# Performance work log

Hardware: AMD Instinct MI355X
Metric: run time of the kernel (lower is better)

The kernel has to match this reference:

```python
import jax, jax.numpy as jnp
import numpy as np

MAX_RADIUS = 0.2
MIN_RADIUS = 0.0
SAMPLE_NUM = 32
CHANNEL = 64
EPS = 1e-5


def _ball_query(points, centers):
    """points (B,N,3), centers (B,M,3) -> idx (B,M,S) int32.
    Mimics pointnet2 ball_query: first SAMPLE_NUM point indices within
    [MIN_RADIUS, MAX_RADIUS); slots past the last found repeat the first
    found index (0 if the ball is empty)."""
    d2 = jnp.sum((centers[:, :, None, :] - points[:, None, :, :]) ** 2, axis=-1)  # (B,M,N)
    mask = (d2 < MAX_RADIUS ** 2) & (d2 >= MIN_RADIUS ** 2)
    N = points.shape[1]
    scores = jnp.where(mask, jnp.arange(N, dtype=jnp.int32), jnp.int32(N))
    neg_vals, _ = jax.lax.top_k(-scores, SAMPLE_NUM)  # k smallest indices
    idx = -neg_vals  # (B,M,S), invalid slots == N
    first = idx[..., :1]
    first = jnp.where(first == N, 0, first)
    idx = jnp.where(idx == N, first, idx)
    return idx


def setup_inputs() -> dict:
    key = jax.random.key(0)
    k1, k2, k3, k4 = jax.random.split(key, 4)
    B, N, M, C = 4, 16384, 2048, CHANNEL
    return {
        "points_xyz": jax.random.uniform(k1, (B, N, 3), dtype=jnp.float32),
        "center_xyz": jax.random.uniform(k2, (B, M, 3), dtype=jnp.float32),
        "center_feature": jax.random.normal(k3, (B, M, C), dtype=jnp.float32),
        "features": jax.random.normal(k4, (B, C, N), dtype=jnp.float32),
        "affine_alpha": jnp.ones((1, 1, 1, C + 3), dtype=jnp.float32),
        "affine_beta": jnp.zeros((1, 1, 1, C + 3), dtype=jnp.float32),
    }


def reference(points_xyz, center_xyz, center_feature, features, affine_alpha, affine_beta):
    idx = _ball_query(points_xyz, center_xyz)  # (B,M,S)
    gather = jax.vmap(lambda a, i: a[i])  # per-batch fancy gather
    grouped_xyz = gather(points_xyz, idx)                      # (B,M,S,3)
    grouped_feat = gather(jnp.swapaxes(features, 1, 2), idx)   # (B,M,S,C)
    nf = jnp.concatenate([grouped_xyz, grouped_feat], axis=-1)  # (B,M,S,3+C)
    mean = jnp.concatenate([center_xyz, center_feature], axis=-1)[:, :, None, :]
    centered = nf - mean
    B = nf.shape[0]
    # torch.std default: unbiased (ddof=1), one scalar per batch element
    std = jnp.std(centered.reshape(B, -1), axis=-1, ddof=1).reshape(B, 1, 1, 1)
    out = affine_alpha * (centered / (std + EPS)) + affine_beta  # (B,M,S,3+C)
    return jnp.transpose(out, (0, 3, 1, 2))  # (B,3+C,M,S)
```

## Files before the change

kernel.cpp:

```cpp
#include <hip/hip_runtime.h>
#include <cstdint>
#include <cstddef>

#define B_ 4
#define N_ 16384
#define M_ 2048
#define C_ 64
#define S_ 32
#define J_ 67
#define R2_ 0.04f
#define EPS_ 1e-5f

__global__ __launch_bounds__(256) void k_phase1(
        const float* __restrict__ feat, float* __restrict__ featT,
        const float* __restrict__ pts, const float* __restrict__ ctr,
        int* __restrict__ idx_ws) {
    __shared__ float tile[64][65];
    int blk = blockIdx.x;
    int tid = threadIdx.x;

    if (blk < 1024) {
        int b  = blk >> 8;
        int n0 = (blk & 255) << 6;
        int r = tid >> 6, i = tid & 63;
        const float* fb = feat + (size_t)b * C_ * N_;
        #pragma unroll
        for (int cc = r; cc < 64; cc += 4)
            tile[cc][i] = fb[(size_t)cc * N_ + n0 + i];
        __syncthreads();
        float* ftb = featT + (size_t)b * N_ * C_;
        #pragma unroll
        for (int nn = r; nn < 64; nn += 4)
            ftb[(size_t)(n0 + nn) * C_ + i] = tile[i][nn];
        return;
    }

    int* sidx = (int*)&tile[0][0];
    int w    = tid >> 6;
    int lane = tid & 63;
    int bm   = (blk - 1024) * 4 + w;
    int b    = bm >> 11;
    const float* pb = pts + (size_t)b * N_ * 3;
    float cx = ctr[(size_t)bm * 3 + 0];
    float cy = ctr[(size_t)bm * 3 + 1];
    float cz = ctr[(size_t)bm * 3 + 2];

    float xs[4], ys[4], zs[4], xn[4], yn[4], zn[4];
    #pragma unroll
    for (int r = 0; r < 4; r++) {
        int i = r * 64 + lane;
        xs[r] = pb[i * 3 + 0]; ys[r] = pb[i * 3 + 1]; zs[r] = pb[i * 3 + 2];
    }
    int cnt = 0;
    for (int base = 0; base < N_; base += 256) {
        int nxt = base + 256;
        if (nxt < N_) {
            #pragma unroll
            for (int r = 0; r < 4; r++) {
                int i = nxt + r * 64 + lane;
                xn[r] = pb[i * 3 + 0]; yn[r] = pb[i * 3 + 1]; zn[r] = pb[i * 3 + 2];
            }
        }
        #pragma unroll
        for (int r = 0; r < 4; r++) {
            float dx = __fsub_rn(cx, xs[r]);
            float dy = __fsub_rn(cy, ys[r]);
            float dz = __fsub_rn(cz, zs[r]);
            float d2 = __fadd_rn(__fadd_rn(__fmul_rn(dx, dx), __fmul_rn(dy, dy)),
                                 __fmul_rn(dz, dz));
            bool in = d2 < R2_;
            unsigned long long mk = __ballot(in);
            int rank = __popcll(mk & ((1ull << lane) - 1ull));
            int pos = cnt + rank;
            if (in && pos < S_) sidx[w * S_ + pos] = base + r * 64 + lane;
            cnt += __popcll(mk);
            if (cnt >= S_) break;
        }
        if (cnt >= S_ || nxt >= N_) break;
        #pragma unroll
        for (int r = 0; r < 4; r++) { xs[r] = xn[r]; ys[r] = yn[r]; zs[r] = zn[r]; }
    }
    __syncthreads();
    int cfound = cnt < S_ ? cnt : S_;
    if (lane < S_) {
        int first = (cfound > 0) ? sidx[w * S_] : 0;
        int v = (lane < cfound) ? sidx[w * S_ + lane] : first;
        idx_ws[(size_t)bm * S_ + lane] = v;
    }
}

__global__ __launch_bounds__(256) void k_sums(
        const float* __restrict__ pts, const float* __restrict__ ctr,
        const float* __restrict__ featT, const float* __restrict__ cfeat,
        const int* __restrict__ idx_ws, float* __restrict__ bpart) {
    __shared__ float pp1[8], pp2[8];
    int w    = threadIdx.x >> 6;
    int lane = threadIdx.x & 63;
    #pragma unroll
    for (int cc = 0; cc < 2; cc++) {
        int ci = w * 2 + cc;
        int bm = blockIdx.x * 8 + ci;
        int b  = bm >> 11;
        const float* pb  = pts + (size_t)b * N_ * 3;
        const float* ftb = featT + (size_t)b * N_ * C_;
        int id = idx_ws[(size_t)bm * S_ + (lane & 31)];
        float cf = cfeat[(size_t)bm * C_ + lane];
        float cx = ctr[(size_t)bm * 3 + 0];
        float cy = ctr[(size_t)bm * 3 + 1];
        float cz = ctr[(size_t)bm * 3 + 2];

        float s1 = 0.f, s2 = 0.f;
        float v[S_];
        #pragma unroll
        for (int s = 0; s < S_; s++) {
            int p = __shfl(id, s);
            v[s] = ftb[(size_t)p * C_ + lane];
        }
        #pragma unroll
        for (int s = 0; s < S_; s++) { float d = v[s] - cf; s1 += d; s2 += d * d; }
        float cj = (lane < 32) ? cx : cy;
        float pv = pb[id * 3 + (lane >> 5)];
        float d0 = pv - cj; s1 += d0; s2 += d0 * d0;
        if (lane < 32) { float dz = pb[id * 3 + 2] - cz; s1 += dz; s2 += dz * dz; }
        #pragma unroll
        for (int off = 32; off > 0; off >>= 1) {
            s1 += __shfl_down(s1, off);
            s2 += __shfl_down(s2, off);
        }
        if (lane == 0) { pp1[ci] = s1; pp2[ci] = s2; }
    }
    __syncthreads();
    if (threadIdx.x == 0) {
        float a1 = 0.f, a2 = 0.f;
        #pragma unroll
        for (int i = 0; i < 8; i++) { a1 += pp1[i]; a2 += pp2[i]; }
        bpart[blockIdx.x * 2 + 0] = a1;
        bpart[blockIdx.x * 2 + 1] = a2;
    }
}

__global__ __launch_bounds__(256) void k_output(
        const float* __restrict__ pts, const float* __restrict__ ctr,
        const float* __restrict__ featT, const float* __restrict__ cfeat,
        const float* __restrict__ alpha, const float* __restrict__ beta,
        const int* __restrict__ idx_ws, const float* __restrict__ bpart,
        float* __restrict__ out) {
    __shared__ float r1[256], r2[256];
    int blk = blockIdx.x, tid = threadIdx.x;
    int batch = blk >> 8;

    const float* bp = bpart + (size_t)batch * 256 * 2;
    r1[tid] = bp[tid * 2 + 0];
    r2[tid] = bp[tid * 2 + 1];
    __syncthreads();
    for (int off = 128; off > 0; off >>= 1) {
        if (tid < off) { r1[tid] += r1[tid + off]; r2[tid] += r2[tid + off]; }
        __syncthreads();
    }
    float sum = r1[0], sumsq = r2[0];
    const float n = (float)(M_ * S_ * J_);
    float mean = sum / n;
    float var  = (sumsq - sum * mean) / (n - 1.f);
    float inv  = 1.f / (sqrtf(var) + EPS_);

    int mi = tid >> 5;
    int cg = (tid >> 3) & 3;
    int sq = tid & 7;
    int m  = (blk & 255) * 8 + mi;
    int s0 = sq * 4;
    size_t bm = (size_t)batch * M_ + m;
    int4 pidx = *(const int4*)(idx_ws + bm * S_ + s0);
    const float* pb = pts + (size_t)batch * N_ * 3;
    size_t obase = ((size_t)batch * J_ * M_ + m) * (size_t)S_ + s0;

    if (cg == 0) {
        #pragma unroll
        for (int j = 0; j < 3; j++) {
            float a = alpha[j] * inv, bt = beta[j];
            float cj = ctr[bm * 3 + j];
            float4 o;
            o.x = a * (pb[pidx.x * 3 + j] - cj) + bt;
            o.y = a * (pb[pidx.y * 3 + j] - cj) + bt;
            o.z = a * (pb[pidx.z * 3 + j] - cj) + bt;
            o.w = a * (pb[pidx.w * 3 + j] - cj) + bt;
            *(float4*)(out + obase + (size_t)j * (M_ * S_)) = o;
        }
    }
    const float4* f0 = (const float4*)(featT + ((size_t)batch * N_ + pidx.x) * C_);
    const float4* f1 = (const float4*)(featT + ((size_t)batch * N_ + pidx.y) * C_);
    const float4* f2 = (const float4*)(featT + ((size_t)batch * N_ + pidx.z) * C_);
    const float4* f3 = (const float4*)(featT + ((size_t)batch * N_ + pidx.w) * C_);
    const float4* cf = (const float4*)(cfeat + bm * C_);
    #pragma unroll
    for (int cq = cg * 4; cq < cg * 4 + 4; cq++) {
        float4 v0 = f0[cq], v1 = f1[cq], v2 = f2[cq], v3 = f3[cq], c = cf[cq];
        int j = 3 + cq * 4;
        float a0 = alpha[j + 0] * inv, b0 = beta[j + 0];
        float a1 = alpha[j + 1] * inv, b1 = beta[j + 1];
        float a2 = alpha[j + 2] * inv, b2 = beta[j + 2];
        float a3 = alpha[j + 3] * inv, b3 = beta[j + 3];
        float4 o0, o1, o2, o3;
        o0.x = a0 * (v0.x - c.x) + b0; o0.y = a0 * (v1.x - c.x) + b0;
        o0.z = a0 * (v2.x - c.x) + b0; o0.w = a0 * (v3.x - c.x) + b0;
        o1.x = a1 * (v0.y - c.y) + b1; o1.y = a1 * (v1.y - c.y) + b1;
        o1.z = a1 * (v2.y - c.y) + b1; o1.w = a1 * (v3.y - c.y) + b1;
        o2.x = a2 * (v0.z - c.z) + b2; o2.y = a2 * (v1.z - c.z) + b2;
        o2.z = a2 * (v2.z - c.z) + b2; o2.w = a2 * (v3.z - c.z) + b2;
        o3.x = a3 * (v0.w - c.w) + b3; o3.y = a3 * (v1.w - c.w) + b3;
        o3.z = a3 * (v2.w - c.w) + b3; o3.w = a3 * (v3.w - c.w) + b3;
        *(float4*)(out + obase + (size_t)(j + 0) * (M_ * S_)) = o0;
        *(float4*)(out + obase + (size_t)(j + 1) * (M_ * S_)) = o1;
        *(float4*)(out + obase + (size_t)(j + 2) * (M_ * S_)) = o2;
        *(float4*)(out + obase + (size_t)(j + 3) * (M_ * S_)) = o3;
    }
}

extern "C" void kernel_launch(void* const* d_in, const int* in_sizes, int n_in,
                              void* d_out, int out_size, void* d_ws, size_t ws_size,
                              hipStream_t stream) {
    const float* pts   = (const float*)d_in[0];
    const float* ctr   = (const float*)d_in[1];
    const float* cfeat = (const float*)d_in[2];
    const float* feat  = (const float*)d_in[3];
    const float* alpha = (const float*)d_in[4];
    const float* beta  = (const float*)d_in[5];
    float* out = (float*)d_out;

    char* ws = (char*)d_ws;
    float* featT = (float*)ws;
    int*   idx_ws = (int*)(ws + (size_t)B_ * N_ * C_ * 4);
    float* bpart = (float*)(ws + (size_t)B_ * N_ * C_ * 4 + (size_t)B_ * M_ * S_ * 4);

    k_phase1<<<3072, 256, 0, stream>>>(feat, featT, pts, ctr, idx_ws);
    k_sums<<<B_ * M_ / 8, 256, 0, stream>>>(pts, ctr, featT, cfeat, idx_ws, bpart);
    k_output<<<1024, 256, 0, stream>>>(pts, ctr, featT, cfeat, alpha, beta,
                                       idx_ws, bpart, out);
}
```

Baseline: 48.93 us.

## Split ball-query scan for each center across four waves of a block

Each block now handles one center, with four waves scanning interleaved 256-point chunks of a 1024-point window and merging their hits in order through shared memory. This shortens the serial per-wave scan chain that limited ball-query latency. In exchange, it launches four times as many blocks, adds two block barriers per window, and always scans full 1024-point windows.

Result: no change. 48.75 us (-0.4%).

```diff
diff --git a/kernel.cpp b/kernel.cpp
--- a/kernel.cpp
+++ b/kernel.cpp
@@ -35,10 +35,12 @@
         return;
     }
 
-    int* sidx = (int*)&tile[0][0];
+    __shared__ int wcnt[4];
+    __shared__ int widx[4][S_];
+    __shared__ int result[S_];
     int w    = tid >> 6;
     int lane = tid & 63;
-    int bm   = (blk - 1024) * 4 + w;
+    int bm   = blk - 1024;
     int b    = bm >> 11;
     const float* pb = pts + (size_t)b * N_ * 3;
     float cx = ctr[(size_t)bm * 3 + 0];
@@ -48,19 +50,21 @@
     float xs[4], ys[4], zs[4], xn[4], yn[4], zn[4];
     #pragma unroll
     for (int r = 0; r < 4; r++) {
-        int i = r * 64 + lane;
+        int i = w * 256 + r * 64 + lane;
         xs[r] = pb[i * 3 + 0]; ys[r] = pb[i * 3 + 1]; zs[r] = pb[i * 3 + 2];
     }
-    int cnt = 0;
-    for (int base = 0; base < N_; base += 256) {
-        int nxt = base + 256;
-        if (nxt < N_) {
+    int total = 0;
+    for (int base = 0; base < N_; base += 1024) {
+        int nb = base + 1024;
+        if (nb < N_) {
             #pragma unroll
             for (int r = 0; r < 4; r++) {
-                int i = nxt + r * 64 + lane;
+                int i = nb + w * 256 + r * 64 + lane;
                 xn[r] = pb[i * 3 + 0]; yn[r] = pb[i * 3 + 1]; zn[r] = pb[i * 3 + 2];
             }
         }
+        int cbase = base + w * 256;
+        int cnt = 0;
         #pragma unroll
         for (int r = 0; r < 4; r++) {
             float dx = __fsub_rn(cx, xs[r]);
@@ -72,20 +76,29 @@
             unsigned long long mk = __ballot(in);
             int rank = __popcll(mk & ((1ull << lane) - 1ull));
             int pos = cnt + rank;
-            if (in && pos < S_) sidx[w * S_ + pos] = base + r * 64 + lane;
+            if (in && pos < S_) widx[w][pos] = cbase + r * 64 + lane;
             cnt += __popcll(mk);
-            if (cnt >= S_) break;
-        }
-        if (cnt >= S_ || nxt >= N_) break;
+        }
+        if (lane == 0) wcnt[w] = cnt;
+        __syncthreads();
+        int c0 = wcnt[0], c1 = wcnt[1], c2 = wcnt[2], c3 = wcnt[3];
+        int offw = total + ((w > 0) ? c0 : 0) + ((w > 1) ? c1 : 0) + ((w > 2) ? c2 : 0);
+        int cw = wcnt[w] < S_ ? wcnt[w] : S_;
+        if (lane < cw) {
+            int dst = offw + lane;
+            if (dst < S_) result[dst] = widx[w][lane];
+        }
+        __syncthreads();
+        total += c0 + c1 + c2 + c3;
+        if (total >= S_ || nb >= N_) break;
         #pragma unroll
         for (int r = 0; r < 4; r++) { xs[r] = xn[r]; ys[r] = yn[r]; zs[r] = zn[r]; }
     }
-    __syncthreads();
-    int cfound = cnt < S_ ? cnt : S_;
-    if (lane < S_) {
-        int first = (cfound > 0) ? sidx[w * S_] : 0;
-        int v = (lane < cfound) ? sidx[w * S_ + lane] : first;
-        idx_ws[(size_t)bm * S_ + lane] = v;
+    int cfound = total < S_ ? total : S_;
+    if (tid < S_) {
+        int first = (cfound > 0) ? result[0] : 0;
+        int v = (tid < cfound) ? result[tid] : first;
+        idx_ws[(size_t)bm * S_ + tid] = v;
     }
 }
 
@@ -231,7 +244,7 @@
     int*   idx_ws = (int*)(ws + (size_t)B_ * N_ * C_ * 4);
     float* bpart = (float*)(ws + (size_t)B_ * N_ * C_ * 4 + (size_t)B_ * M_ * S_ * 4);
 
-    k_phase1<<<3072, 256, 0, stream>>>(feat, featT, pts, ctr, idx_ws);
+    k_phase1<<<1024 + B_ * M_, 256, 0, stream>>>(feat, featT, pts, ctr, idx_ws);
     k_sums<<<B_ * M_ / 8, 256, 0, stream>>>(pts, ctr, featT, cfeat, idx_ws, bpart);
     k_output<<<1024, 256, 0, stream>>>(pts, ctr, featT, cfeat, alpha, beta,
                                        idx_ws, bpart, out);
```
